# Kernel tuning notes

Hardware: AMD Instinct MI355X
Metric: run time of the kernel (lower is better)

Reference implementation:

```python
import jax, jax.numpy as jnp
import numpy as np

N_NODES = 50000
N_EDGES = 600000
IN_DIM = 128
HID = 128


def setup_inputs() -> dict:
    key = jax.random.key(0)
    ks = jax.random.split(key, 8)
    x = jax.random.normal(ks[0], (N_NODES, IN_DIM), dtype=jnp.float32)
    edge_index = jax.random.randint(ks[1], (2, N_EDGES), 0, N_NODES, dtype=jnp.int64)
    def lin(k, fan_in, fan_out):
        s = 1.0 / np.sqrt(fan_in)
        kw, kb = jax.random.split(k)
        W = jax.random.uniform(kw, (fan_in, fan_out), jnp.float32, -s, s)
        b = jax.random.uniform(kb, (fan_out,), jnp.float32, -s, s)
        return W, b
    W0, b0 = lin(ks[2], IN_DIM, HID)
    W1, b1 = lin(ks[3], HID, HID)
    W2, b2 = lin(ks[4], HID, HID)
    return {"x": x, "edge_index": edge_index, "W0": W0, "b0": b0,
            "W1": W1, "b1": b1, "W2": W2, "b2": b2}


def reference(x, edge_index, W0, b0, W1, b1, W2, b2):
    n = x.shape[0]
    loops = jnp.arange(n, dtype=edge_index.dtype)
    src = jnp.concatenate([edge_index[0], loops])  # source nodes (+self loops)
    dst = jnp.concatenate([edge_index[1], loops])  # destination nodes
    # symmetric GCN normalization: deg^{-1/2}[src] * deg^{-1/2}[dst]
    deg = jax.ops.segment_sum(jnp.ones(src.shape[0], x.dtype), dst, num_segments=n)
    dinv = jnp.where(deg > 0, jax.lax.rsqrt(deg), 0.0)
    norm = dinv[src] * dinv[dst]  # [E+N]

    def gcn_layer(h, W, b):
        hw = h @ W                              # [N, H]
        msg = hw[src] * norm[:, None]           # gather + scale, [E+N, H]
        agg = jax.ops.segment_sum(msg, dst, num_segments=n)  # scatter-add
        return agg + b

    h = x
    for W, b in ((W0, b0), (W1, b1), (W2, b2)):
        h = jax.nn.relu(gcn_layer(h, W, b))     # dropout is identity in eval
    return h  # JK='last'
```

## Files before the change

### kernel.cpp

```cpp
#include <hip/hip_runtime.h>

#define NN 50000
#define NE 600000
#define DIM 128
#define NB_N 196
#define NB_E2 1172
#define TILES 3125
#define ROWW 136
#define STRIDE 64
#define LOG2S 6

#define CB_CAST0 NB_E2
#define CB_GEMM0 (NB_E2 + 128)
#define NB_GEMM 782
#define NB_CNT (CB_GEMM0 + NB_GEMM)

#define FB_PAD0 NB_E2
#define FB_SENT (NB_E2 + NB_N)
#define FB_SCALE0 (FB_SENT + 1)
#define NB_SCALE 6250
#define NB_FILL (FB_SCALE0 + NB_SCALE)

typedef unsigned short u16;
typedef unsigned int u32;
typedef __attribute__((ext_vector_type(8))) short bf16x8;
typedef __attribute__((ext_vector_type(4))) float f32x4;

__device__ __forceinline__ u16 f2bf(float f) {
    u32 u = __builtin_bit_cast(u32, f);
    u32 r = (u + 0x7FFFu + ((u >> 16) & 1u)) >> 16;
    return (u16)r;
}
__device__ __forceinline__ float bflo(u32 w) { return __builtin_bit_cast(float, w << 16); }
__device__ __forceinline__ float bfhi(u32 w) { return __builtin_bit_cast(float, w & 0xffff0000u); }
__device__ __forceinline__ int pad16(int d) {
    int p = (d + 15) & ~15;
    return p < 16 ? 16 : p;
}

__global__ __launch_bounds__(256) void k_count(const int* __restrict__ ei,
                                               int* __restrict__ deg,
                                               int* __restrict__ rank,
                                               const float* __restrict__ W0,
                                               const float* __restrict__ W1,
                                               const float* __restrict__ W2,
                                               u16* __restrict__ Wt,
                                               const float* __restrict__ x,
                                               float* __restrict__ hF) {
    int b = blockIdx.x;
    if (b < NB_E2) {
        __shared__ int s64;
        if (threadIdx.x == 0) {
            int o = 0;
#pragma unroll
            for (int j = 0; j < 16; j++) o |= ei[2 * j + 1];
            s64 = (o == 0);
        }
        __syncthreads();
        int p = b * 256 + threadIdx.x;
        int ebase = 2 * p;
        if (ebase >= NE) return;
        int d0, d1;
        if (s64) {
            int4 dd = *(const int4*)(ei + 2 * (NE + ebase));
            d0 = dd.x; d1 = dd.z;
        } else {
            int2 dd = *(const int2*)(ei + NE + ebase);
            d0 = dd.x; d1 = dd.y;
        }
        int r0 = atomicAdd(&deg[d0], 1);
        int r1 = atomicAdd(&deg[d1], 1);
        *(int2*)(rank + ebase) = make_int2(r0, r1);
        return;
    }
    if (b < CB_GEMM0) {
        int idx = (b - CB_CAST0) * 256 + threadIdx.x;
        int l = idx >> 14, rem = idx & 16383;
        int n = rem >> 7, k = rem & 127;
        const float* W = (l == 0) ? W1 : W2;
        Wt[16384 + idx] = f2bf(W[k * 128 + n]);
        return;
    }
    int gb = b - CB_GEMM0;
    int lane = threadIdx.x & 63;
    int tile = gb * 4 + (threadIdx.x >> 6);
    if (tile >= TILES) return;
    int r = lane & 15, q = lane >> 4;
    long rowbase = (long)tile * 16;
    bf16x8 Af[4];
#pragma unroll
    for (int kc = 0; kc < 4; kc++) {
        const float4* p = (const float4*)(x + (rowbase + r) * 128 + kc * 32 + q * 8);
        float4 t0 = p[0], t1 = p[1];
        bf16x8 a;
        a[0] = (short)f2bf(t0.x); a[1] = (short)f2bf(t0.y);
        a[2] = (short)f2bf(t0.z); a[3] = (short)f2bf(t0.w);
        a[4] = (short)f2bf(t1.x); a[5] = (short)f2bf(t1.y);
        a[6] = (short)f2bf(t1.z); a[7] = (short)f2bf(t1.w);
        Af[kc] = a;
    }
#pragma unroll
    for (int nt = 0; nt < 8; nt++) {
        bf16x8 Bf[4];
#pragma unroll
        for (int kc = 0; kc < 4; kc++) {
            const float* col = W0 + (size_t)(kc * 32 + q * 8) * 128 + nt * 16 + r;
#pragma unroll
            for (int i = 0; i < 8; i++)
                Bf[kc][i] = (short)f2bf(col[(size_t)i * 128]);
        }
        f32x4 acc = {0.f, 0.f, 0.f, 0.f};
#pragma unroll
        for (int kc = 0; kc < 4; kc++)
            acc = __builtin_amdgcn_mfma_f32_16x16x32_bf16(Af[kc], Bf[kc], acc, 0, 0, 0);
#pragma unroll
        for (int i = 0; i < 4; i++)
            hF[(rowbase + q * 4 + i) * 128 + nt * 16 + r] = acc[i];
    }
}

__global__ __launch_bounds__(256) void k_fill(const int* __restrict__ ei,
                                              const int* __restrict__ deg,
                                              const int* __restrict__ rank,
                                              int* __restrict__ recs,
                                              const float* __restrict__ hF,
                                              u16* __restrict__ hwA,
                                              u16* __restrict__ hwB) {
    int b = blockIdx.x;
    if (b < NB_E2) {
        __shared__ int s64;
        if (threadIdx.x == 0) {
            int o = 0;
#pragma unroll
            for (int j = 0; j < 16; j++) o |= ei[2 * j + 1];
            s64 = (o == 0);
        }
        __syncthreads();
        int p = b * 256 + threadIdx.x;
        int ebase = 2 * p;
        if (ebase >= NE) return;
        int s0, s1, d0, d1;
        if (s64) {
            int4 ss = *(const int4*)(ei + 2 * ebase);
            int4 dd = *(const int4*)(ei + 2 * (NE + ebase));
            s0 = ss.x; s1 = ss.z; d0 = dd.x; d1 = dd.z;
        } else {
            int2 ss = *(const int2*)(ei + ebase);
            int2 dd = *(const int2*)(ei + NE + ebase);
            s0 = ss.x; s1 = ss.y; d0 = dd.x; d1 = dd.y;
        }
        int2 rk = *(const int2*)(rank + ebase);
        recs[(d0 << LOG2S) + rk.x] = s0;
        recs[(d1 << LOG2S) + rk.y] = s1;
        return;
    }
    if (b < FB_SENT) {
        int i = (b - FB_PAD0) * 256 + threadIdx.x;
        if (i < NN) {
            int base = i << LOG2S, d = deg[i], p = pad16(d);
            for (int j = d; j < p; j++) recs[base + j] = NN;
        }
        return;
    }
    if (b == FB_SENT) {
        if (threadIdx.x < 64) {
            ((u32*)(hwA + (size_t)NN * DIM))[threadIdx.x] = 0;
        } else if (threadIdx.x < 128) {
            ((u32*)(hwB + (size_t)NN * DIM))[threadIdx.x - 64] = 0;
        }
        return;
    }
    int idx = (b - FB_SCALE0) * 256 + threadIdx.x;
    int row = idx >> 5, part = idx & 31;
    float dv = rsqrtf((float)(deg[row] + 1));
    float4 v = *(const float4*)(hF + (size_t)row * 128 + part * 4);
    u32 lo = (u32)f2bf(dv * v.x) | ((u32)f2bf(dv * v.y) << 16);
    u32 hi = (u32)f2bf(dv * v.z) | ((u32)f2bf(dv * v.w) << 16);
    *(uint2*)(hwA + (size_t)row * 128 + part * 4) = make_uint2(lo, hi);
}

__device__ __forceinline__ void add8(float* a, uint4 u) {
    a[0] += bflo(u.x); a[1] += bfhi(u.x);
    a[2] += bflo(u.y); a[3] += bfhi(u.y);
    a[4] += bflo(u.z); a[5] += bfhi(u.z);
    a[6] += bflo(u.w); a[7] += bfhi(u.w);
}

__device__ __forceinline__ void agg_pair(const u16* __restrict__ hw,
                                         const int* __restrict__ recs,
                                         int va, int da, int db, int g, int r,
                                         float* A, float* B) {
    int vb = va + 1;
    uint4 sva = *(const uint4*)(hw + (size_t)va * DIM + r * 8);
    uint4 svb = *(const uint4*)(hw + (size_t)vb * DIM + r * 8);
    float m = (g == 0) ? 1.0f : 0.0f;
    A[0] = m * bflo(sva.x); A[1] = m * bfhi(sva.x);
    A[2] = m * bflo(sva.y); A[3] = m * bfhi(sva.y);
    A[4] = m * bflo(sva.z); A[5] = m * bfhi(sva.z);
    A[6] = m * bflo(sva.w); A[7] = m * bfhi(sva.w);
    B[0] = m * bflo(svb.x); B[1] = m * bfhi(svb.x);
    B[2] = m * bflo(svb.y); B[3] = m * bfhi(svb.y);
    B[4] = m * bflo(svb.z); B[5] = m * bfhi(svb.z);
    B[6] = m * bflo(svb.w); B[7] = m * bfhi(svb.w);

    int ea = va << LOG2S, enda = ea + pad16(da);
    int eb = vb << LOG2S, endb = eb + pad16(db);
    const int go = 4 * g;
    int4 qa = *(const int4*)(recs + ea + go);
    int4 qb = *(const int4*)(recs + eb + go);
    while (ea < enda || eb < endb) {
        int sa0 = (ea < enda) ? qa.x : NN;
        int sa1 = (ea < enda) ? qa.y : NN;
        int sa2 = (ea < enda) ? qa.z : NN;
        int sa3 = (ea < enda) ? qa.w : NN;
        int sb0 = (eb < endb) ? qb.x : NN;
        int sb1 = (eb < endb) ? qb.y : NN;
        int sb2 = (eb < endb) ? qb.z : NN;
        int sb3 = (eb < endb) ? qb.w : NN;
        uint4 ua0 = *(const uint4*)(hw + (size_t)(u32)sa0 * DIM + r * 8);
        uint4 ua1 = *(const uint4*)(hw + (size_t)(u32)sa1 * DIM + r * 8);
        uint4 ua2 = *(const uint4*)(hw + (size_t)(u32)sa2 * DIM + r * 8);
        uint4 ua3 = *(const uint4*)(hw + (size_t)(u32)sa3 * DIM + r * 8);
        uint4 ub0 = *(const uint4*)(hw + (size_t)(u32)sb0 * DIM + r * 8);
        uint4 ub1 = *(const uint4*)(hw + (size_t)(u32)sb1 * DIM + r * 8);
        uint4 ub2 = *(const uint4*)(hw + (size_t)(u32)sb2 * DIM + r * 8);
        uint4 ub3 = *(const uint4*)(hw + (size_t)(u32)sb3 * DIM + r * 8);
        ea += 16; eb += 16;
        int4 qa_n = *(const int4*)(recs + min(ea, enda - 16) + go);
        int4 qb_n = *(const int4*)(recs + min(eb, endb - 16) + go);
        add8(A, ua0); add8(A, ua1); add8(A, ua2); add8(A, ua3);
        add8(B, ub0); add8(B, ub1); add8(B, ub2); add8(B, ub3);
        qa = qa_n; qb = qb_n;
    }
}

__device__ __forceinline__ void combine_scale(float dv, const float* bias, int r,
                                              float* acc) {
#pragma unroll
    for (int j = 0; j < 8; j++) {
        acc[j] += __shfl_xor(acc[j], 16, 64);
        acc[j] += __shfl_xor(acc[j], 32, 64);
    }
    float4 b0 = ((const float4*)bias)[2 * r];
    float4 b1 = ((const float4*)bias)[2 * r + 1];
    acc[0] = fmaxf(fmaf(dv, acc[0], b0.x), 0.f);
    acc[1] = fmaxf(fmaf(dv, acc[1], b0.y), 0.f);
    acc[2] = fmaxf(fmaf(dv, acc[2], b0.z), 0.f);
    acc[3] = fmaxf(fmaf(dv, acc[3], b0.w), 0.f);
    acc[4] = fmaxf(fmaf(dv, acc[4], b1.x), 0.f);
    acc[5] = fmaxf(fmaf(dv, acc[5], b1.y), 0.f);
    acc[6] = fmaxf(fmaf(dv, acc[6], b1.z), 0.f);
    acc[7] = fmaxf(fmaf(dv, acc[7], b1.w), 0.f);
}

__global__ __launch_bounds__(256) void k_agg_gemm(const u16* __restrict__ hw_in,
                                                  const int* __restrict__ deg,
                                                  const int* __restrict__ recs,
                                                  const float* __restrict__ bias,
                                                  const u16* __restrict__ Wt,
                                                  u16* __restrict__ hw_out) {
    __shared__ u16 sm[16 * ROWW];
    int lane = threadIdx.x & 63;
    int w = threadIdx.x >> 6;
    int g = lane >> 4, r = lane & 15;
    int base = blockIdx.x * 16;
#pragma unroll
    for (int p = 0; p < 2; p++) {
        int rowa = w * 4 + 2 * p;
        int va = base + rowa;
        int2 dd = *(const int2*)(deg + va);
        float A[8], B[8];
        agg_pair(hw_in, recs, va, dd.x, dd.y, g, r, A, B);
        combine_scale(rsqrtf((float)(dd.x + 1)), bias, r, A);
        combine_scale(rsqrtf((float)(dd.y + 1)), bias, r, B);
        if (g == 0) {
            uint4 pk;
            pk.x = (u32)f2bf(A[0]) | ((u32)f2bf(A[1]) << 16);
            pk.y = (u32)f2bf(A[2]) | ((u32)f2bf(A[3]) << 16);
            pk.z = (u32)f2bf(A[4]) | ((u32)f2bf(A[5]) << 16);
            pk.w = (u32)f2bf(A[6]) | ((u32)f2bf(A[7]) << 16);
            *(uint4*)(sm + rowa * ROWW + r * 8) = pk;
            pk.x = (u32)f2bf(B[0]) | ((u32)f2bf(B[1]) << 16);
            pk.y = (u32)f2bf(B[2]) | ((u32)f2bf(B[3]) << 16);
            pk.z = (u32)f2bf(B[4]) | ((u32)f2bf(B[5]) << 16);
            pk.w = (u32)f2bf(B[6]) | ((u32)f2bf(B[7]) << 16);
            *(uint4*)(sm + (rowa + 1) * ROWW + r * 8) = pk;
        }
    }
    __syncthreads();
    int q = lane >> 4;
    bf16x8 Af[4];
#pragma unroll
    for (int kc = 0; kc < 4; kc++)
        Af[kc] = *(const bf16x8*)(sm + r * ROWW + kc * 32 + q * 8);
    int4 dq = *(const int4*)(deg + base + q * 4);
    float dv[4];
    dv[0] = rsqrtf((float)(dq.x + 1));
    dv[1] = rsqrtf((float)(dq.y + 1));
    dv[2] = rsqrtf((float)(dq.z + 1));
    dv[3] = rsqrtf((float)(dq.w + 1));
#pragma unroll
    for (int t = 0; t < 2; t++) {
        int nt = w * 2 + t;
        f32x4 acc = {0.f, 0.f, 0.f, 0.f};
#pragma unroll
        for (int kc = 0; kc < 4; kc++) {
            bf16x8 Bf = *(const bf16x8*)(Wt + ((nt * 16 + r) << 7) + kc * 32 + q * 8);
            acc = __builtin_amdgcn_mfma_f32_16x16x32_bf16(Af[kc], Bf, acc, 0, 0, 0);
        }
#pragma unroll
        for (int i = 0; i < 4; i++)
            hw_out[(size_t)(base + q * 4 + i) * DIM + nt * 16 + r] = f2bf(dv[i] * acc[i]);
    }
}

__global__ __launch_bounds__(256) void k_agg_out(const u16* __restrict__ hw_in,
                                                 const int* __restrict__ deg,
                                                 const int* __restrict__ recs,
                                                 const float* __restrict__ bias,
                                                 float* __restrict__ out) {
    int lane = threadIdx.x & 63;
    int w = threadIdx.x >> 6;
    int g = lane >> 4, r = lane & 15;
    int va = blockIdx.x * 8 + w * 2;
    int2 dd = *(const int2*)(deg + va);
    float A[8], B[8];
    agg_pair(hw_in, recs, va, dd.x, dd.y, g, r, A, B);
    combine_scale(rsqrtf((float)(dd.x + 1)), bias, r, A);
    combine_scale(rsqrtf((float)(dd.y + 1)), bias, r, B);
    if (g == 0) {
        float4* p = (float4*)(out + (size_t)va * DIM + r * 8);
        p[0] = make_float4(A[0], A[1], A[2], A[3]);
        p[1] = make_float4(A[4], A[5], A[6], A[7]);
        p = (float4*)(out + (size_t)(va + 1) * DIM + r * 8);
        p[0] = make_float4(B[0], B[1], B[2], B[3]);
        p[1] = make_float4(B[4], B[5], B[6], B[7]);
    }
}


extern "C" void kernel_launch(void* const* d_in, const int* in_sizes, int n_in,
                              void* d_out, int out_size, void* d_ws, size_t ws_size,
                              hipStream_t stream) {
    const float* x = (const float*)d_in[0];
    const int* ei = (const int*)d_in[1];
    const float* W0 = (const float*)d_in[2];
    const float* b0 = (const float*)d_in[3];
    const float* W1 = (const float*)d_in[4];
    const float* b1 = (const float*)d_in[5];
    const float* W2 = (const float*)d_in[6];
    const float* b2 = (const float*)d_in[7];

    char* ws = (char*)d_ws;
    size_t off = 0;
    auto alloc = [&](size_t bytes) -> void* {
        void* p = ws + off;
        off += (bytes + 511) & ~(size_t)511;
        return p;
    };
    int* deg = (int*)alloc(NN * 4);
    size_t zbytes = off;
    int* rank = (int*)alloc((size_t)NE * 4);
    int* recs = (int*)alloc((size_t)NN * STRIDE * 4 + 512);
    u16* Wt = (u16*)alloc(3 * 128 * 128 * 2);
    u16* hwA = (u16*)alloc((size_t)(NN + 1) * DIM * 2);
    u16* hwB = (u16*)alloc((size_t)(NN + 1) * DIM * 2);
    float* hF = (float*)alloc((size_t)NN * DIM * 4);

    hipMemsetAsync(ws, 0, zbytes, stream);
    k_count<<<NB_CNT, 256, 0, stream>>>(ei, deg, rank, W0, W1, W2, Wt, x, hF);
    k_fill<<<NB_FILL, 256, 0, stream>>>(ei, deg, rank, recs, hF, hwA, hwB);
    k_agg_gemm<<<TILES, 256, 0, stream>>>(hwA, deg, recs, b0, Wt + 16384, hwB);
    k_agg_gemm<<<TILES, 256, 0, stream>>>(hwB, deg, recs, b1, Wt + 32768, hwA);
    k_agg_out<<<6250, 256, 0, stream>>>(hwA, deg, recs, b2, (float*)d_out);
}
```

Before: 243.7 us.

## Move layer-0 GEMM into fill kernel and fuse degree scaling, drop fp32 staging

The first-layer X·W0 GEMM moves from the count kernel into the fill kernel, which runs after degrees are known. The deg^-1/2 scaling and bf16 store to hwA now happen in the GEMM epilogue, so the fp32 hF intermediate and its separate scale pass go away. W0 is pre-transposed to bf16 alongside W1 and W2, so the B fragments are loaded as vectors instead of strided fp32 reads. The trade-off is that the GEMM no longer overlaps with the atomic degree counting, and the epilogue writes scattered 2-byte stores.

```diff
diff --git a/kernel.cpp b/kernel.cpp
--- a/kernel.cpp
+++ b/kernel.cpp
@@ -10,16 +10,13 @@
 #define STRIDE 64
 #define LOG2S 6
 
-#define CB_CAST0 NB_E2
-#define CB_GEMM0 (NB_E2 + 128)
-#define NB_GEMM 782
-#define NB_CNT (CB_GEMM0 + NB_GEMM)
+#define NB_CNT (NB_E2 + 192)
 
 #define FB_PAD0 NB_E2
 #define FB_SENT (NB_E2 + NB_N)
-#define FB_SCALE0 (FB_SENT + 1)
-#define NB_SCALE 6250
-#define NB_FILL (FB_SCALE0 + NB_SCALE)
+#define FB_GEMM0 (FB_SENT + 1)
+#define NB_GEMM 782
+#define NB_FILL (FB_GEMM0 + NB_GEMM)
 
 typedef unsigned short u16;
 typedef unsigned int u32;
@@ -44,86 +41,46 @@
                                                const float* __restrict__ W0,
                                                const float* __restrict__ W1,
                                                const float* __restrict__ W2,
-                                               u16* __restrict__ Wt,
-                                               const float* __restrict__ x,
-                                               float* __restrict__ hF) {
+                                               u16* __restrict__ Wt) {
     int b = blockIdx.x;
-    if (b < NB_E2) {
-        __shared__ int s64;
-        if (threadIdx.x == 0) {
-            int o = 0;
-#pragma unroll
-            for (int j = 0; j < 16; j++) o |= ei[2 * j + 1];
-            s64 = (o == 0);
-        }
-        __syncthreads();
-        int p = b * 256 + threadIdx.x;
-        int ebase = 2 * p;
-        if (ebase >= NE) return;
-        int d0, d1;
-        if (s64) {
-            int4 dd = *(const int4*)(ei + 2 * (NE + ebase));
-            d0 = dd.x; d1 = dd.z;
-        } else {
-            int2 dd = *(const int2*)(ei + NE + ebase);
-            d0 = dd.x; d1 = dd.y;
-        }
-        int r0 = atomicAdd(&deg[d0], 1);
-        int r1 = atomicAdd(&deg[d1], 1);
-        *(int2*)(rank + ebase) = make_int2(r0, r1);
-        return;
-    }
-    if (b < CB_GEMM0) {
-        int idx = (b - CB_CAST0) * 256 + threadIdx.x;
+    if (b >= NB_E2) {
+        int idx = (b - NB_E2) * 256 + threadIdx.x;
         int l = idx >> 14, rem = idx & 16383;
         int n = rem >> 7, k = rem & 127;
-        const float* W = (l == 0) ? W1 : W2;
-        Wt[16384 + idx] = f2bf(W[k * 128 + n]);
+        const float* W = (l == 0) ? W0 : ((l == 1) ? W1 : W2);
+        Wt[idx] = f2bf(W[k * 128 + n]);
         return;
     }
-    int gb = b - CB_GEMM0;
-    int lane = threadIdx.x & 63;
-    int tile = gb * 4 + (threadIdx.x >> 6);
-    if (tile >= TILES) return;
-    int r = lane & 15, q = lane >> 4;
-    long rowbase = (long)tile * 16;
-    bf16x8 Af[4];
-#pragma unroll
-    for (int kc = 0; kc < 4; kc++) {
-        const float4* p = (const float4*)(x + (rowbase + r) * 128 + kc * 32 + q * 8);
-        float4 t0 = p[0], t1 = p[1];
-        bf16x8 a;
-        a[0] = (short)f2bf(t0.x); a[1] = (short)f2bf(t0.y);
-        a[2] = (short)f2bf(t0.z); a[3] = (short)f2bf(t0.w);
-        a[4] = (short)f2bf(t1.x); a[5] = (short)f2bf(t1.y);
-        a[6] = (short)f2bf(t1.z); a[7] = (short)f2bf(t1.w);
-        Af[kc] = a;
-    }
-#pragma unroll
-    for (int nt = 0; nt < 8; nt++) {
-        bf16x8 Bf[4];
-#pragma unroll
-        for (int kc = 0; kc < 4; kc++) {
-            const float* col = W0 + (size_t)(kc * 32 + q * 8) * 128 + nt * 16 + r;
-#pragma unroll
-            for (int i = 0; i < 8; i++)
-                Bf[kc][i] = (short)f2bf(col[(size_t)i * 128]);
-        }
-        f32x4 acc = {0.f, 0.f, 0.f, 0.f};
-#pragma unroll
-        for (int kc = 0; kc < 4; kc++)
-            acc = __builtin_amdgcn_mfma_f32_16x16x32_bf16(Af[kc], Bf[kc], acc, 0, 0, 0);
-#pragma unroll
-        for (int i = 0; i < 4; i++)
-            hF[(rowbase + q * 4 + i) * 128 + nt * 16 + r] = acc[i];
-    }
+    __shared__ int s64;
+    if (threadIdx.x == 0) {
+        int o = 0;
+#pragma unroll
+        for (int j = 0; j < 16; j++) o |= ei[2 * j + 1];
+        s64 = (o == 0);
+    }
+    __syncthreads();
+    int p = b * 256 + threadIdx.x;
+    int ebase = 2 * p;
+    if (ebase >= NE) return;
+    int d0, d1;
+    if (s64) {
+        int4 dd = *(const int4*)(ei + 2 * (NE + ebase));
+        d0 = dd.x; d1 = dd.z;
+    } else {
+        int2 dd = *(const int2*)(ei + NE + ebase);
+        d0 = dd.x; d1 = dd.y;
+    }
+    int r0 = atomicAdd(&deg[d0], 1);
+    int r1 = atomicAdd(&deg[d1], 1);
+    *(int2*)(rank + ebase) = make_int2(r0, r1);
 }
 
 __global__ __launch_bounds__(256) void k_fill(const int* __restrict__ ei,
                                               const int* __restrict__ deg,
                                               const int* __restrict__ rank,
                                               int* __restrict__ recs,
-                                              const float* __restrict__ hF,
+                                              const float* __restrict__ x,
+                                              const u16* __restrict__ Wt,
                                               u16* __restrict__ hwA,
                                               u16* __restrict__ hwB) {
     int b = blockIdx.x;
@@ -170,13 +127,42 @@
         }
         return;
     }
-    int idx = (b - FB_SCALE0) * 256 + threadIdx.x;
-    int row = idx >> 5, part = idx & 31;
-    float dv = rsqrtf((float)(deg[row] + 1));
-    float4 v = *(const float4*)(hF + (size_t)row * 128 + part * 4);
-    u32 lo = (u32)f2bf(dv * v.x) | ((u32)f2bf(dv * v.y) << 16);
-    u32 hi = (u32)f2bf(dv * v.z) | ((u32)f2bf(dv * v.w) << 16);
-    *(uint2*)(hwA + (size_t)row * 128 + part * 4) = make_uint2(lo, hi);
+    int gb = b - FB_GEMM0;
+    int lane = threadIdx.x & 63;
+    int tile = gb * 4 + (threadIdx.x >> 6);
+    if (tile >= TILES) return;
+    int r = lane & 15, q = lane >> 4;
+    long rowbase = (long)tile * 16;
+    bf16x8 Af[4];
+#pragma unroll
+    for (int kc = 0; kc < 4; kc++) {
+        const float4* p = (const float4*)(x + (rowbase + r) * 128 + kc * 32 + q * 8);
+        float4 t0 = p[0], t1 = p[1];
+        bf16x8 a;
+        a[0] = (short)f2bf(t0.x); a[1] = (short)f2bf(t0.y);
+        a[2] = (short)f2bf(t0.z); a[3] = (short)f2bf(t0.w);
+        a[4] = (short)f2bf(t1.x); a[5] = (short)f2bf(t1.y);
+        a[6] = (short)f2bf(t1.z); a[7] = (short)f2bf(t1.w);
+        Af[kc] = a;
+    }
+    int4 dq = *(const int4*)(deg + rowbase + q * 4);
+    float dv[4];
+    dv[0] = rsqrtf((float)(dq.x + 1));
+    dv[1] = rsqrtf((float)(dq.y + 1));
+    dv[2] = rsqrtf((float)(dq.z + 1));
+    dv[3] = rsqrtf((float)(dq.w + 1));
+#pragma unroll
+    for (int nt = 0; nt < 8; nt++) {
+        f32x4 acc = {0.f, 0.f, 0.f, 0.f};
+#pragma unroll
+        for (int kc = 0; kc < 4; kc++) {
+            bf16x8 Bf = *(const bf16x8*)(Wt + ((nt * 16 + r) << 7) + kc * 32 + q * 8);
+            acc = __builtin_amdgcn_mfma_f32_16x16x32_bf16(Af[kc], Bf, acc, 0, 0, 0);
+        }
+#pragma unroll
+        for (int i = 0; i < 4; i++)
+            hwA[(rowbase + q * 4 + i) * 128 + nt * 16 + r] = f2bf(dv[i] * acc[i]);
+    }
 }
 
 __device__ __forceinline__ void add8(float* a, uint4 u) {
@@ -365,11 +351,10 @@
     u16* Wt = (u16*)alloc(3 * 128 * 128 * 2);
     u16* hwA = (u16*)alloc((size_t)(NN + 1) * DIM * 2);
     u16* hwB = (u16*)alloc((size_t)(NN + 1) * DIM * 2);
-    float* hF = (float*)alloc((size_t)NN * DIM * 4);
 
     hipMemsetAsync(ws, 0, zbytes, stream);
-    k_count<<<NB_CNT, 256, 0, stream>>>(ei, deg, rank, W0, W1, W2, Wt, x, hF);
-    k_fill<<<NB_FILL, 256, 0, stream>>>(ei, deg, rank, recs, hF, hwA, hwB);
+    k_count<<<NB_CNT, 256, 0, stream>>>(ei, deg, rank, W0, W1, W2, Wt);
+    k_fill<<<NB_FILL, 256, 0, stream>>>(ei, deg, rank, recs, x, Wt, hwA, hwB);
     k_agg_gemm<<<TILES, 256, 0, stream>>>(hwA, deg, recs, b0, Wt + 16384, hwB);
     k_agg_gemm<<<TILES, 256, 0, stream>>>(hwB, deg, recs, b1, Wt + 32768, hwA);
     k_agg_out<<<6250, 256, 0, stream>>>(hwA, deg, recs, b2, (float*)d_out);
```

Result: no change. 244.5 us (+0.3%).
